# Optimization experiments

Hardware: AMD Instinct MI355X
Metric: run time of the kernel (lower is better)

## Reference

```python
import jax, jax.numpy as jnp
import numpy as np

N_NODES = 50000
N_EDGES = 800000
N_GRAPHS = 512
F_IN = 9
H = 64
H2 = 32


def gcn_conv(x, W, b, edge_index, num_nodes):
    # PyG GCNConv: add self loops, sym-normalize, x @ W, scatter-add, + bias
    src, dst = edge_index[0], edge_index[1]
    xw = x @ W  # [N, out]
    deg = 1.0 + jax.ops.segment_sum(jnp.ones_like(src, dtype=xw.dtype), dst,
                                    num_segments=num_nodes)  # self-loop adds 1
    dis = jax.lax.rsqrt(deg)  # deg >= 1
    norm = dis[src] * dis[dst]  # [E]
    out = jax.ops.segment_sum(xw[src] * norm[:, None], dst, num_segments=num_nodes)
    out = out + xw * (dis * dis)[:, None]  # self-loop contribution
    return out + b


def edge_conv(x, W, b, edge_index, num_nodes):
    # PyG EdgeConv with nn = Linear(2*in, out) + ReLU, aggr='max'
    src, dst = edge_index[0], edge_index[1]
    xi = x[dst]
    xj = x[src]
    h = jax.nn.relu(jnp.concatenate([xi, xj - xi], axis=-1) @ W + b)  # [E, out]
    agg = jax.ops.segment_max(h, dst, num_segments=num_nodes)
    return jnp.where(jnp.isfinite(agg), agg, 0.0)  # empty segments -> 0


def setup_inputs() -> dict:
    key = jax.random.key(0)
    ks = jax.random.split(key, 16)
    x = jax.random.normal(ks[0], (N_NODES, F_IN), dtype=jnp.float32)
    edge_index = jax.random.randint(ks[1], (2, N_EDGES), 0, N_NODES, dtype=jnp.int32)
    adj = jax.random.randint(ks[2], (2, N_EDGES), 0, N_NODES, dtype=jnp.int32)
    batch = jnp.sort(jax.random.randint(ks[3], (N_NODES,), 0, N_GRAPHS, dtype=jnp.int32))
    s = lambda fan_in: 1.0 / np.sqrt(fan_in)
    W1 = jax.random.uniform(ks[4], (F_IN, H), jnp.float32, -s(F_IN), s(F_IN))
    b1 = jnp.zeros((H,), jnp.float32)
    eW1 = jax.random.uniform(ks[5], (2 * H, H), jnp.float32, -s(2 * H), s(2 * H))
    eb1 = jnp.zeros((H,), jnp.float32)
    W2 = jax.random.uniform(ks[6], (H, H2), jnp.float32, -s(H), s(H))
    b2 = jnp.zeros((H2,), jnp.float32)
    eW2 = jax.random.uniform(ks[7], (2 * H2, H2), jnp.float32, -s(2 * H2), s(2 * H2))
    eb2 = jnp.zeros((H2,), jnp.float32)
    fcW = jax.random.uniform(ks[8], (H2, 1), jnp.float32, -s(H2), s(H2))
    fcb = jax.random.uniform(ks[9], (1,), jnp.float32, -s(H2), s(H2))
    return {"x": x, "edge_index": edge_index, "adj": adj, "batch": batch,
            "W1": W1, "b1": b1, "eW1": eW1, "eb1": eb1,
            "W2": W2, "b2": b2, "eW2": eW2, "eb2": eb2,
            "fcW": fcW, "fcb": fcb}


def reference(x, edge_index, adj, batch, W1, b1, eW1, eb1, W2, b2, eW2, eb2, fcW, fcb):
    n = x.shape[0]
    h = jax.nn.relu(gcn_conv(x, W1, b1, edge_index, n))
    h = jax.nn.relu(edge_conv(h, eW1, eb1, adj, n))
    h = jax.nn.relu(gcn_conv(h, W2, b2, edge_index, n))
    h = jax.nn.relu(edge_conv(h, eW2, eb2, adj, n))
    h = h @ fcW + fcb  # [N, 1]
    # global_mean_pool
    sums = jax.ops.segment_sum(h, batch, num_segments=N_GRAPHS)
    cnts = jax.ops.segment_sum(jnp.ones((n, 1), h.dtype), batch, num_segments=N_GRAPHS)
    return sums / jnp.maximum(cnts, 1.0)
```

## Files before the change

kernel.cpp:

```cpp
#include <hip/hip_runtime.h>
#include <math.h>

#define NN 50000
#define NE 800000
#define NG 512
#define FIN 9
#define D1 64
#define D2 32
#define PAD 64
#define NN2 (2 * NN)

static inline int cdiv(int a, int b) { return (a + b - 1) / b; }

__global__ void k_build(const int* __restrict__ ei, const int* __restrict__ adj,
                        int* __restrict__ head_e, int* __restrict__ next_e,
                        int* __restrict__ head_a, int* __restrict__ next_a) {
  int e = blockIdx.x * blockDim.x + threadIdx.x;
  if (e < NE) {
    int d1 = ei[NE + e];
    next_e[e] = atomicExch(&head_e[d1], e);
    int d2 = adj[NE + e];
    next_a[e] = atomicExch(&head_a[d2], e);
  }
}

__global__ void k_convert(const int* __restrict__ head_e, const int* __restrict__ next_e,
                          const int* __restrict__ head_a, const int* __restrict__ next_a,
                          const int* __restrict__ ei, const int* __restrict__ adj,
                          int* __restrict__ deg_e, int* __restrict__ slot_e,
                          int* __restrict__ deg_a, int* __restrict__ slot_a) {
  int t = blockIdx.x * blockDim.x + threadIdx.x;
  if (t >= NN2) return;
  bool isE = t < NN;
  int i = isE ? t : t - NN;
  int e = isE ? head_e[i] : head_a[i];
  const int* nxt = isE ? next_e : next_a;
  const int* sv = isE ? ei : adj;
  int* slot = (isE ? slot_e : slot_a) + (size_t)i * PAD;
  int p = 0;
  while (e >= 0 && p < PAD) {
    slot[p++] = sv[e];
    e = nxt[e];
  }
  (isE ? deg_e : deg_a)[i] = p;
}

__global__ void k_xw1(const float* __restrict__ x, const float* __restrict__ W1,
                      const int* __restrict__ deg_e, float* __restrict__ dis,
                      float* __restrict__ xws1) {
  int gid = blockIdx.x * blockDim.x + threadIdx.x;
  int i = gid >> 6, j = gid & 63;
  if (i >= NN) return;
  float di = rsqrtf(1.0f + (float)deg_e[i]);
  if (j == 0) dis[i] = di;
  const float* xr = x + i * FIN;
  float acc = 0.f;
#pragma unroll
  for (int k = 0; k < FIN; ++k) acc += xr[k] * W1[k * D1 + j];
  xws1[i * D1 + j] = acc * di;
}

template <int FI, int FOT, int MODE, bool SCALE>
__global__ __launch_bounds__(256) void k_gemm(const float* __restrict__ H,
                                              const float* __restrict__ W,
                                              const float* __restrict__ dis,
                                              float* __restrict__ OA,
                                              float* __restrict__ OB) {
  constexpr int TM = 4;
  constexpr int TN = (FOT >= 64) ? 4 : 2;
  constexpr int BN = 1024 * TN / FOT;
  constexpr int LDH = BN + 1;
  constexpr int FO = FOT / 2;
  __shared__ float ht[FI][LDH];
  __shared__ float wc[FI][FOT];

  for (int t = threadIdx.x; t < FI * FOT; t += 256) {
    int k = t / FOT, j = t % FOT;
    float v;
    if (MODE == 1)
      v = (j < FO) ? W[k * FO + j] : W[(FI + k) * FO + (j - FO)];
    else
      v = W[k * FOT + j];
    wc[k][j] = v;
  }
  int node0 = blockIdx.x * BN;
  for (int t = threadIdx.x; t < BN * FI; t += 256) {
    int n = t / FI, k = t % FI;
    int nn = node0 + n;
    ht[k][n] = (nn < NN) ? H[(size_t)nn * FI + k] : 0.f;
  }
  __syncthreads();

  int tn = threadIdx.x % (FOT / TN);
  int tm = threadIdx.x / (FOT / TN);
  int j0 = tn * TN, n0 = tm * TM;

  float acc[TM][TN];
#pragma unroll
  for (int m = 0; m < TM; ++m)
#pragma unroll
    for (int q = 0; q < TN; ++q) acc[m][q] = 0.f;

  for (int k = 0; k < FI; ++k) {
    float wv[TN];
    if (TN == 4) {
      float4 w4 = *(const float4*)&wc[k][j0];
      wv[0] = w4.x; wv[1] = w4.y; wv[2] = w4.z; wv[3] = w4.w;
    } else {
      float2 w2 = *(const float2*)&wc[k][j0];
      wv[0] = w2.x; wv[1] = w2.y;
    }
    float hv[TM];
#pragma unroll
    for (int m = 0; m < TM; ++m) hv[m] = ht[k][n0 + m];
#pragma unroll
    for (int m = 0; m < TM; ++m)
#pragma unroll
      for (int q = 0; q < TN; ++q) acc[m][q] += hv[m] * wv[q];
  }

#pragma unroll
  for (int m = 0; m < TM; ++m) {
    int n = node0 + n0 + m;
    if (n >= NN) break;
    float sc = SCALE ? dis[n] : 1.0f;
    float* dst;
    if (MODE == 1)
      dst = (j0 < FO) ? (OA + (size_t)n * FO + j0) : (OB + (size_t)n * FO + (j0 - FO));
    else
      dst = OA + (size_t)n * FOT + j0;
    if (TN == 4) {
      float4 o = {acc[m][0] * sc, acc[m][1] * sc, acc[m][2] * sc, acc[m][3] * sc};
      *(float4*)dst = o;
    } else {
      float2 o = {acc[m][0] * sc, acc[m][1] * sc};
      *(float2*)dst = o;
    }
  }
}

template <int F>
__global__ void k_gcn4(const float4* __restrict__ xws, const float* __restrict__ dis,
                       const int* __restrict__ deg, const int* __restrict__ slots,
                       const float* __restrict__ b, float4* __restrict__ hout) {
  constexpr int L = F / 4;
  int gid = blockIdx.x * blockDim.x + threadIdx.x;
  int i = gid / L, l = gid % L;
  if (i >= NN) return;
  const int* s = slots + (size_t)i * PAD;
  int n = deg[i];
  float4 acc = xws[(size_t)i * L + l];
  int t = 0;
  for (; t + 7 < n; t += 8) {
    int i0 = s[t], i1 = s[t + 1], i2 = s[t + 2], i3 = s[t + 3];
    int i4 = s[t + 4], i5 = s[t + 5], i6 = s[t + 6], i7 = s[t + 7];
    float4 v0 = xws[(size_t)i0 * L + l];
    float4 v1 = xws[(size_t)i1 * L + l];
    float4 v2 = xws[(size_t)i2 * L + l];
    float4 v3 = xws[(size_t)i3 * L + l];
    float4 v4 = xws[(size_t)i4 * L + l];
    float4 v5 = xws[(size_t)i5 * L + l];
    float4 v6 = xws[(size_t)i6 * L + l];
    float4 v7 = xws[(size_t)i7 * L + l];
    acc.x += ((v0.x + v1.x) + (v2.x + v3.x)) + ((v4.x + v5.x) + (v6.x + v7.x));
    acc.y += ((v0.y + v1.y) + (v2.y + v3.y)) + ((v4.y + v5.y) + (v6.y + v7.y));
    acc.z += ((v0.z + v1.z) + (v2.z + v3.z)) + ((v4.z + v5.z) + (v6.z + v7.z));
    acc.w += ((v0.w + v1.w) + (v2.w + v3.w)) + ((v4.w + v5.w) + (v6.w + v7.w));
  }
  for (; t < n; ++t) {
    float4 v = xws[(size_t)s[t] * L + l];
    acc.x += v.x; acc.y += v.y; acc.z += v.z; acc.w += v.w;
  }
  float di = dis[i];
  float4 bb = ((const float4*)b)[l];
  float4 o;
  o.x = fmaxf(bb.x + di * acc.x, 0.f);
  o.y = fmaxf(bb.y + di * acc.y, 0.f);
  o.z = fmaxf(bb.z + di * acc.z, 0.f);
  o.w = fmaxf(bb.w + di * acc.w, 0.f);
  hout[(size_t)i * L + l] = o;
}

template <int F>
__global__ void k_edge4(const float4* __restrict__ A, const float4* __restrict__ B,
                        const float* __restrict__ eb, const int* __restrict__ deg,
                        const int* __restrict__ slots, float4* __restrict__ hout) {
  constexpr int L = F / 4;
  int gid = blockIdx.x * blockDim.x + threadIdx.x;
  int i = gid / L, l = gid % L;
  if (i >= NN) return;
  const int* s = slots + (size_t)i * PAD;
  int n = deg[i];
  float4 M = {-INFINITY, -INFINITY, -INFINITY, -INFINITY};
  int t = 0;
  for (; t + 7 < n; t += 8) {
    int i0 = s[t], i1 = s[t + 1], i2 = s[t + 2], i3 = s[t + 3];
    int i4 = s[t + 4], i5 = s[t + 5], i6 = s[t + 6], i7 = s[t + 7];
    float4 v0 = B[(size_t)i0 * L + l];
    float4 v1 = B[(size_t)i1 * L + l];
    float4 v2 = B[(size_t)i2 * L + l];
    float4 v3 = B[(size_t)i3 * L + l];
    float4 v4 = B[(size_t)i4 * L + l];
    float4 v5 = B[(size_t)i5 * L + l];
    float4 v6 = B[(size_t)i6 * L + l];
    float4 v7 = B[(size_t)i7 * L + l];
    M.x = fmaxf(M.x, fmaxf(fmaxf(fmaxf(v0.x, v1.x), fmaxf(v2.x, v3.x)),
                           fmaxf(fmaxf(v4.x, v5.x), fmaxf(v6.x, v7.x))));
    M.y = fmaxf(M.y, fmaxf(fmaxf(fmaxf(v0.y, v1.y), fmaxf(v2.y, v3.y)),
                           fmaxf(fmaxf(v4.y, v5.y), fmaxf(v6.y, v7.y))));
    M.z = fmaxf(M.z, fmaxf(fmaxf(fmaxf(v0.z, v1.z), fmaxf(v2.z, v3.z)),
                           fmaxf(fmaxf(v4.z, v5.z), fmaxf(v6.z, v7.z))));
    M.w = fmaxf(M.w, fmaxf(fmaxf(fmaxf(v0.w, v1.w), fmaxf(v2.w, v3.w)),
                           fmaxf(fmaxf(v4.w, v5.w), fmaxf(v6.w, v7.w))));
  }
  for (; t < n; ++t) {
    float4 v = B[(size_t)s[t] * L + l];
    M.x = fmaxf(M.x, v.x); M.y = fmaxf(M.y, v.y);
    M.z = fmaxf(M.z, v.z); M.w = fmaxf(M.w, v.w);
  }
  float4 a = A[(size_t)i * L + l];
  float4 bsl = B[(size_t)i * L + l];
  float4 e4 = ((const float4*)eb)[l];
  float4 o;
  o.x = fmaxf(a.x - bsl.x + e4.x + M.x, 0.f);
  o.y = fmaxf(a.y - bsl.y + e4.y + M.y, 0.f);
  o.z = fmaxf(a.z - bsl.z + e4.z + M.z, 0.f);
  o.w = fmaxf(a.w - bsl.w + e4.w + M.w, 0.f);
  hout[(size_t)i * L + l] = o;
}

__global__ void k_final(const float* __restrict__ h4, const float* __restrict__ fcW,
                        const float* __restrict__ fcb, const int* __restrict__ batch,
                        float* __restrict__ sums, float* __restrict__ cnt) {
  int i = blockIdx.x * blockDim.x + threadIdx.x;
  int lane = threadIdx.x & 63;
  bool valid = (i < NN);
  float val = 0.f, c = 0.f;
  int g = -1;
  if (valid) {
    float acc = fcb[0];
#pragma unroll
    for (int k = 0; k < D2; ++k) acc += h4[(size_t)i * D2 + k] * fcW[k];
    val = acc;
    c = 1.f;
    g = batch[i];
  }
#pragma unroll
  for (int d = 1; d < 64; d <<= 1) {
    float v2 = __shfl_down(val, d);
    float c2 = __shfl_down(c, d);
    int g2 = __shfl_down(g, d);
    if (lane + d < 64 && g2 == g) {
      val += v2;
      c += c2;
    }
  }
  int gprev = __shfl_up(g, 1);
  bool is_head = (lane == 0) || (gprev != g);
  if (valid && is_head) {
    atomicAdd(&sums[g], val);
    atomicAdd(&cnt[g], c);
  }
}

__global__ void k_out(const float* __restrict__ sums, const float* __restrict__ cnt,
                      float* __restrict__ out) {
  int g = blockIdx.x * blockDim.x + threadIdx.x;
  if (g < NG) out[g] = sums[g] / fmaxf(cnt[g], 1.0f);
}

extern "C" void kernel_launch(void* const* d_in, const int* in_sizes, int n_in,
                              void* d_out, int out_size, void* d_ws, size_t ws_size,
                              hipStream_t stream) {
  const float* x = (const float*)d_in[0];
  const int* ei = (const int*)d_in[1];
  const int* adj = (const int*)d_in[2];
  const int* batch = (const int*)d_in[3];
  const float* W1 = (const float*)d_in[4];
  const float* b1 = (const float*)d_in[5];
  const float* eW1 = (const float*)d_in[6];
  const float* eb1 = (const float*)d_in[7];
  const float* W2 = (const float*)d_in[8];
  const float* b2 = (const float*)d_in[9];
  const float* eW2 = (const float*)d_in[10];
  const float* eb2 = (const float*)d_in[11];
  const float* fcW = (const float*)d_in[12];
  const float* fcb = (const float*)d_in[13];
  float* out = (float*)d_out;

  char* ws = (char*)d_ws;
  size_t p = 0;
  auto alloc = [&](size_t bytes) -> void* {
    void* r = ws + p;
    p = (p + bytes + 255) & ~(size_t)255;
    return r;
  };
  int* head_e = (int*)alloc(NN * 4);
  int* head_a = (int*)alloc(NN * 4);
  size_t ff_bytes = p;
  float* sums = (float*)alloc(NG * 4);
  float* cnt = (float*)alloc(NG * 4);
  size_t zero_end = p;
  int* next_e = (int*)alloc(NE * 4);
  int* next_a = (int*)alloc(NE * 4);
  int* deg_e = (int*)alloc(NN * 4);
  int* deg_a = (int*)alloc(NN * 4);
  int* slot_e = (int*)alloc((size_t)NN * PAD * 4);
  int* slot_a = (int*)alloc((size_t)NN * PAD * 4);
  float* dis = (float*)alloc(NN * 4);
  float* buf0 = (float*)alloc((size_t)NN * D1 * 4);
  float* buf1 = (float*)alloc((size_t)NN * D1 * 4);
  float* buf2 = (float*)alloc((size_t)NN * D1 * 4);
  float* buf3 = (float*)alloc((size_t)NN * D1 * 4);

  hipMemsetAsync(d_ws, 0xFF, ff_bytes, stream);
  hipMemsetAsync(ws + ff_bytes, 0, zero_end - ff_bytes, stream);

  k_build<<<cdiv(NE, 256), 256, 0, stream>>>(ei, adj, head_e, next_e, head_a, next_a);
  k_convert<<<cdiv(NN2, 256), 256, 0, stream>>>(head_e, next_e, head_a, next_a, ei, adj,
                                                deg_e, slot_e, deg_a, slot_a);

  k_xw1<<<cdiv(NN * D1, 256), 256, 0, stream>>>(x, W1, deg_e, dis, buf0);
  k_gcn4<D1><<<cdiv(NN * (D1 / 4), 256), 256, 0, stream>>>(
      (const float4*)buf0, dis, deg_e, slot_e, b1, (float4*)buf1);

  k_gemm<D1, 2 * D1, 1, false><<<cdiv(NN, 32), 256, 0, stream>>>(buf1, eW1, nullptr, buf2, buf3);
  k_edge4<D1><<<cdiv(NN * (D1 / 4), 256), 256, 0, stream>>>(
      (const float4*)buf2, (const float4*)buf3, eb1, deg_a, slot_a, (float4*)buf0);

  k_gemm<D1, D2, 0, true><<<cdiv(NN, 64), 256, 0, stream>>>(buf0, W2, dis, buf1, nullptr);
  k_gcn4<D2><<<cdiv(NN * (D2 / 4), 256), 256, 0, stream>>>(
      (const float4*)buf1, dis, deg_e, slot_e, b2, (float4*)buf3);

  float* A2 = buf2;
  float* B2 = buf2 + (size_t)NN * D2;
  k_gemm<D2, 2 * D2, 1, false><<<cdiv(NN, 64), 256, 0, stream>>>(buf3, eW2, nullptr, A2, B2);
  k_edge4<D2><<<cdiv(NN * (D2 / 4), 256), 256, 0, stream>>>(
      (const float4*)A2, (const float4*)B2, eb2, deg_a, slot_a, (float4*)buf1);

  k_final<<<cdiv(NN, 256), 256, 0, stream>>>(buf1, fcW, fcb, batch, sums, cnt);
  k_out<<<cdiv(NG, 256), 256, 0, stream>>>(sums, cnt, out);
}
```

Measured before the change: 388.4 us.

## Pack edge source with next pointer and slice gather kernels by feature chunk

Measured after the change: 586.3 us. 50.9% more time.

```diff
diff --git a/kernel.cpp b/kernel.cpp
--- a/kernel.cpp
+++ b/kernel.cpp
@@ -10,23 +10,27 @@
 #define PAD 64
 #define NN2 (2 * NN)
 
+typedef unsigned long long ull;
+
 static inline int cdiv(int a, int b) { return (a + b - 1) / b; }
 
 __global__ void k_build(const int* __restrict__ ei, const int* __restrict__ adj,
-                        int* __restrict__ head_e, int* __restrict__ next_e,
-                        int* __restrict__ head_a, int* __restrict__ next_a) {
+                        int* __restrict__ head_e, ull* __restrict__ pack_e,
+                        int* __restrict__ head_a, ull* __restrict__ pack_a) {
   int e = blockIdx.x * blockDim.x + threadIdx.x;
   if (e < NE) {
-    int d1 = ei[NE + e];
-    next_e[e] = atomicExch(&head_e[d1], e);
-    int d2 = adj[NE + e];
-    next_a[e] = atomicExch(&head_a[d2], e);
-  }
-}
-
-__global__ void k_convert(const int* __restrict__ head_e, const int* __restrict__ next_e,
-                          const int* __restrict__ head_a, const int* __restrict__ next_a,
-                          const int* __restrict__ ei, const int* __restrict__ adj,
+    int s = ei[e], d = ei[NE + e];
+    int nx = atomicExch(&head_e[d], e);
+    pack_e[e] = ((ull)(unsigned)s << 32) | (unsigned)nx;
+    s = adj[e];
+    d = adj[NE + e];
+    nx = atomicExch(&head_a[d], e);
+    pack_a[e] = ((ull)(unsigned)s << 32) | (unsigned)nx;
+  }
+}
+
+__global__ void k_convert(const int* __restrict__ head_e, const ull* __restrict__ pack_e,
+                          const int* __restrict__ head_a, const ull* __restrict__ pack_a,
                           int* __restrict__ deg_e, int* __restrict__ slot_e,
                           int* __restrict__ deg_a, int* __restrict__ slot_a) {
   int t = blockIdx.x * blockDim.x + threadIdx.x;
@@ -34,13 +38,13 @@
   bool isE = t < NN;
   int i = isE ? t : t - NN;
   int e = isE ? head_e[i] : head_a[i];
-  const int* nxt = isE ? next_e : next_a;
-  const int* sv = isE ? ei : adj;
+  const ull* pk = isE ? pack_e : pack_a;
   int* slot = (isE ? slot_e : slot_a) + (size_t)i * PAD;
   int p = 0;
   while (e >= 0 && p < PAD) {
-    slot[p++] = sv[e];
-    e = nxt[e];
+    ull v = pk[e];
+    slot[p++] = (int)(v >> 32);
+    e = (int)(unsigned)(v & 0xffffffffu);
   }
   (isE ? deg_e : deg_a)[i] = p;
 }
@@ -139,14 +143,19 @@
   }
 }
 
-template <int F>
-__global__ void k_gcn4(const float4* __restrict__ xws, const float* __restrict__ dis,
-                       const int* __restrict__ deg, const int* __restrict__ slots,
-                       const float* __restrict__ b, float4* __restrict__ hout) {
+
+template <int F, int NS>
+__global__ void k_gcn4s(const float4* __restrict__ xws, const float* __restrict__ dis,
+                        const int* __restrict__ deg, const int* __restrict__ slots,
+                        const float* __restrict__ b, float4* __restrict__ hout) {
   constexpr int L = F / 4;
-  int gid = blockIdx.x * blockDim.x + threadIdx.x;
-  int i = gid / L, l = gid % L;
+  constexpr int LS = L / NS;
+  constexpr int NB = 256 / LS;
+  int slice = blockIdx.x % NS;
+  int chunk = blockIdx.x / NS;
+  int i = chunk * NB + threadIdx.x / LS;
   if (i >= NN) return;
+  int l = slice * LS + threadIdx.x % LS;
   const int* s = slots + (size_t)i * PAD;
   int n = deg[i];
   float4 acc = xws[(size_t)i * L + l];
@@ -181,14 +190,18 @@
   hout[(size_t)i * L + l] = o;
 }
 
-template <int F>
-__global__ void k_edge4(const float4* __restrict__ A, const float4* __restrict__ B,
-                        const float* __restrict__ eb, const int* __restrict__ deg,
-                        const int* __restrict__ slots, float4* __restrict__ hout) {
+template <int F, int NS>
+__global__ void k_edge4s(const float4* __restrict__ A, const float4* __restrict__ B,
+                         const float* __restrict__ eb, const int* __restrict__ deg,
+                         const int* __restrict__ slots, float4* __restrict__ hout) {
   constexpr int L = F / 4;
-  int gid = blockIdx.x * blockDim.x + threadIdx.x;
-  int i = gid / L, l = gid % L;
+  constexpr int LS = L / NS;
+  constexpr int NB = 256 / LS;
+  int slice = blockIdx.x % NS;
+  int chunk = blockIdx.x / NS;
+  int i = chunk * NB + threadIdx.x / LS;
   if (i >= NN) return;
+  int l = slice * LS + threadIdx.x % LS;
   const int* s = slots + (size_t)i * PAD;
   int n = deg[i];
   float4 M = {-INFINITY, -INFINITY, -INFINITY, -INFINITY};
@@ -301,8 +314,8 @@
   float* sums = (float*)alloc(NG * 4);
   float* cnt = (float*)alloc(NG * 4);
   size_t zero_end = p;
-  int* next_e = (int*)alloc(NE * 4);
-  int* next_a = (int*)alloc(NE * 4);
+  ull* pack_e = (ull*)alloc((size_t)NE * 8);
+  ull* pack_a = (ull*)alloc((size_t)NE * 8);
   int* deg_e = (int*)alloc(NN * 4);
   int* deg_a = (int*)alloc(NN * 4);
   int* slot_e = (int*)alloc((size_t)NN * PAD * 4);
@@ -316,26 +329,29 @@
   hipMemsetAsync(d_ws, 0xFF, ff_bytes, stream);
   hipMemsetAsync(ws + ff_bytes, 0, zero_end - ff_bytes, stream);
 
-  k_build<<<cdiv(NE, 256), 256, 0, stream>>>(ei, adj, head_e, next_e, head_a, next_a);
-  k_convert<<<cdiv(NN2, 256), 256, 0, stream>>>(head_e, next_e, head_a, next_a, ei, adj,
+  k_build<<<cdiv(NE, 256), 256, 0, stream>>>(ei, adj, head_e, pack_e, head_a, pack_a);
+  k_convert<<<cdiv(NN2, 256), 256, 0, stream>>>(head_e, pack_e, head_a, pack_a,
                                                 deg_e, slot_e, deg_a, slot_a);
 
+  const int G64 = 8 * cdiv(NN, 128);
+  const int G32 = 4 * cdiv(NN, 128);
+
   k_xw1<<<cdiv(NN * D1, 256), 256, 0, stream>>>(x, W1, deg_e, dis, buf0);
-  k_gcn4<D1><<<cdiv(NN * (D1 / 4), 256), 256, 0, stream>>>(
+  k_gcn4s<D1, 8><<<G64, 256, 0, stream>>>(
       (const float4*)buf0, dis, deg_e, slot_e, b1, (float4*)buf1);
 
   k_gemm<D1, 2 * D1, 1, false><<<cdiv(NN, 32), 256, 0, stream>>>(buf1, eW1, nullptr, buf2, buf3);
-  k_edge4<D1><<<cdiv(NN * (D1 / 4), 256), 256, 0, stream>>>(
+  k_edge4s<D1, 8><<<G64, 256, 0, stream>>>(
       (const float4*)buf2, (const float4*)buf3, eb1, deg_a, slot_a, (float4*)buf0);
 
   k_gemm<D1, D2, 0, true><<<cdiv(NN, 64), 256, 0, stream>>>(buf0, W2, dis, buf1, nullptr);
-  k_gcn4<D2><<<cdiv(NN * (D2 / 4), 256), 256, 0, stream>>>(
+  k_gcn4s<D2, 4><<<G32, 256, 0, stream>>>(
       (const float4*)buf1, dis, deg_e, slot_e, b2, (float4*)buf3);
 
   float* A2 = buf2;
   float* B2 = buf2 + (size_t)NN * D2;
   k_gemm<D2, 2 * D2, 1, false><<<cdiv(NN, 64), 256, 0, stream>>>(buf3, eW2, nullptr, A2, B2);
-  k_edge4<D2><<<cdiv(NN * (D2 / 4), 256), 256, 0, stream>>>(
+  k_edge4s<D2, 4><<<G32, 256, 0, stream>>>(
       (const float4*)A2, (const float4*)B2, eb2, deg_a, slot_a, (float4*)buf1);
 
   k_final<<<cdiv(NN, 256), 256, 0, stream>>>(buf1, fcW, fcb, batch, sums, cnt);
```
